# Optimization experiments

Hardware: AMD Instinct MI355X
Metric: run time of the kernel (lower is better)

## Reference

```python
import jax, jax.numpy as jnp
import numpy as np

N, BS, T, D = 512, 64, 200, 32
ALPHA, EPS, TIME_LOG, POWER = 0.1, 1e-6, 5.0, 3


def setup_inputs() -> dict:
    key = jax.random.key(0)
    ks = jax.random.split(key, 16)
    s = 0.1
    skills = jax.random.randint(ks[0], (BS, T), 0, N)
    times = jnp.sort(jax.random.randint(ks[1], (BS, T), 0, 100000), axis=1)
    labels = jax.random.uniform(ks[2], (BS, T), dtype=jnp.float32)
    adj = jax.random.uniform(ks[3], (1, BS, N, N), dtype=jnp.float32)
    node_embeddings = jax.random.normal(ks[4], (1, N, 2 * D), dtype=jnp.float32)
    user_b0 = jax.random.uniform(ks[5], (BS, D), dtype=jnp.float32)
    user_f0 = jax.random.uniform(ks[6], (BS, D), dtype=jnp.float32)
    conv1_w = jax.random.normal(ks[7], (D, D, 5), dtype=jnp.float32) * s
    conv1_b = jax.random.normal(ks[8], (D,), dtype=jnp.float32) * s
    conv2_w = jax.random.normal(ks[9], (D, D, 1), dtype=jnp.float32) * s
    conv2_b = jax.random.normal(ks[10], (D,), dtype=jnp.float32) * s
    lin_f_w = jax.random.normal(ks[11], (D, D), dtype=jnp.float32) * s
    lin_f_b = jax.random.normal(ks[12], (D,), dtype=jnp.float32) * s
    lin_b_w = jax.random.normal(ks[13], (D, D), dtype=jnp.float32) * s
    lin_b_b = jax.random.normal(ks[14], (D,), dtype=jnp.float32) * s
    return dict(skills=skills, times=times, labels=labels, adj=adj,
                node_embeddings=node_embeddings, user_b0=user_b0, user_f0=user_f0,
                conv1_w=conv1_w, conv1_b=conv1_b, conv2_w=conv2_w, conv2_b=conv2_b,
                lin_f_w=lin_f_w, lin_f_b=lin_f_b, lin_b_w=lin_b_w, lin_b_b=lin_b_b)


def _forward(skills, times, labels, adj, node_embeddings, user_b0, user_f0,
             conv1_w, conv1_b, conv2_w, conv2_b, lin_f_w, lin_f_b, lin_b_w, lin_b_b):
    n = jnp.float32(N)
    A1 = adj[0]                      # [BS, N, N]  (leading A=1 dim squeezed)
    A2 = jnp.matmul(A1, A1)
    A3 = jnp.matmul(A2, A1)
    # adj^i / N^i for i=1..3, stacked over power dim -> [BS, 3, N, N]
    adj_list = jnp.stack([A1 / n, A2 / (n * n), A3 / (n * n * n)], axis=1)
    node_emb = node_embeddings[0]    # [N, 2D]
    node_send, node_rec = node_emb[:, :D], node_emb[:, D:]
    # temporal deltas: log(|t_i - t_{i-1}| + EPS) / log(time_log) -> [T-1, BS]
    dt = jnp.abs(times[:, 1:] - times[:, :-1]).astype(jnp.float32)
    delta = (jnp.log(dt + EPS) / jnp.log(jnp.float32(TIME_LOG))).T

    last_perf0 = user_b0 @ node_rec.T           # [BS, N]
    node_last_forget0 = user_f0 @ node_send.T   # [BS, N]

    def step(carry, xs):
        user_b, user_f, last_perf, node_last_forget = carry
        delta_t, label_t, skill_t = xs
        node_cur_base = user_b @ node_rec.T                               # [BS, N]
        temporal = jnp.exp(-delta_t[:, None] * ALPHA * node_last_forget) * last_perf
        # sum over powers folded into the contraction; /(power*N) as in source
        spatial = jnp.einsum('bj,bnjk->bk', last_perf, adj_list) / (POWER * n)
        cur_perf = jax.nn.sigmoid(node_cur_base + temporal + spatial)     # [BS, N]
        nlf = user_f @ node_send.T
        lab = jnp.broadcast_to(label_t[:, None], (BS, D))
        user = jnp.stack([user_b, user_f, lab,
                          node_rec[skill_t], node_send[skill_t]], axis=-1)  # [BS, D, 5]
        h = jax.nn.relu(jnp.einsum('bcl,ocl->bo', user, conv1_w) + conv1_b)
        uu = h @ conv2_w[:, :, 0].T + conv2_b
        new_f = jnp.tanh(uu @ lin_f_w.T + lin_f_b)
        new_b = jnp.tanh(uu @ lin_b_w.T + lin_b_b)
        pred = jnp.take_along_axis(cur_perf, skill_t[:, None], axis=1)    # [BS, 1]
        return (new_b, new_f, cur_perf, nlf), pred

    xs = (delta, labels[:, 1:].T, skills[:, 1:].T)
    _, preds = jax.lax.scan(step, (user_b0, user_f0, last_perf0, node_last_forget0), xs)
    return preds  # [T-1, BS, 1]


def reference(skills, times, labels, adj, node_embeddings, user_b0, user_f0,
              conv1_w, conv1_b, conv2_w, conv2_b, lin_f_w, lin_f_b, lin_b_w, lin_b_b):
    return _forward(skills, times, labels, adj, node_embeddings, user_b0, user_f0,
                    conv1_w, conv1_b, conv2_w, conv2_b, lin_f_w, lin_f_b, lin_b_w, lin_b_b)
```

## Files before the change

### kernel.cpp

```cpp
#include <hip/hip_runtime.h>

#define NN 512
#define BSZ 64
#define TTOT 200
#define NSTEP 199
#define DD 32

typedef __attribute__((ext_vector_type(8))) short bf16x8;
typedef __attribute__((ext_vector_type(8))) int i32x8;
typedef __attribute__((ext_vector_type(4))) float f32x4;
typedef __attribute__((ext_vector_type(4))) unsigned int u32x4;

__device__ __forceinline__ float bf2f(unsigned short u) {
  union { unsigned int i; float f; } v; v.i = ((unsigned int)u) << 16; return v.f;
}
__device__ __forceinline__ unsigned short f2bf(float f) {
  unsigned int b = __float_as_uint(f);
  return (unsigned short)((b + 0x7fffu + ((b >> 16) & 1u)) >> 16);
}
__device__ __forceinline__ unsigned int pk_trunc(float hi, float lo) {
  return __builtin_amdgcn_perm(__float_as_uint(hi), __float_as_uint(lo), 0x07060302u);
}
__device__ __forceinline__ unsigned char e4m3(float x) {
  float a = fabsf(x);
  unsigned int s = (__float_as_uint(x) >> 24) & 0x80u;
  if (a < 0.01171875f) return (unsigned char)s;
  a = fminf(a, 448.0f);
  unsigned int u = __float_as_uint(a);
  unsigned int keep = (u >> 20) & 7u;
  unsigned int rest = u & 0xFFFFFu;
  unsigned int base = (((u >> 23) - 120u) << 3) | keep;
  unsigned int rnd = (rest > 0x80000u) || (rest == 0x80000u && (keep & 1u));
  return (unsigned char)(s | (base + rnd));
}
__device__ __forceinline__ float dec8(unsigned char x) {
  int e = (x >> 3) & 15, m = x & 7;
  float v = e ? ldexpf(8.f + (float)m, e - 10) : ldexpf((float)m, -9);
  return (x & 0x80) ? -v : v;
}
__device__ __forceinline__ float rlane(float v, int l) {
  return __int_as_float(__builtin_amdgcn_readlane(__float_as_int(v), l));
}

__device__ __forceinline__ size_t m8_addr(int k, int col) {
  int nt = col >> 4, cch = k >> 5;
  int l2 = (((k >> 3) & 3) << 4) + (col & 15);
  return (size_t)((nt * 16 + cch) * 512) + (size_t)l2 * 8 + (size_t)(k & 7);
}
__device__ __forceinline__ size_t m8mxa(int k, int col) {
  int f = ((k >> 7) << 5) + (col >> 4);
  int ln2 = (((k >> 5) & 3) << 4) + (col & 15);
  return (((size_t)f * 64 + ln2) << 5) + (size_t)(k & 31);
}

__global__ __launch_bounds__(256) void transpose_kernel(
    const float* __restrict__ A1, unsigned short* __restrict__ A1T) {
  const int b = blockIdx.z, ct = blockIdx.x * 64, rt = blockIdx.y * 64;
  const int t = threadIdx.x;
  __shared__ unsigned int tl[64][33];
  {
    const int rp = t >> 3, cs = (t & 7) * 8;
    const float* p0 = A1 + (size_t)b * NN * NN + (size_t)(rt + 2 * rp) * NN + ct + cs;
    f32x4 a0 = *(const f32x4*)p0, a1 = *(const f32x4*)(p0 + 4);
    f32x4 b0 = *(const f32x4*)(p0 + NN), b1 = *(const f32x4*)(p0 + NN + 4);
#pragma unroll
    for (int j = 0; j < 4; ++j) {
      tl[cs + j][rp] = pk_trunc(b0[j], a0[j]);
      tl[cs + 4 + j][rp] = pk_trunc(b1[j], a1[j]);
    }
  }
  __syncthreads();
  {
    const int c = t >> 2, rps = (t & 3) * 8;
    unsigned int v[8];
#pragma unroll
    for (int j = 0; j < 8; ++j) v[j] = tl[c][rps + j];
    unsigned int* dst = (unsigned int*)(A1T + (size_t)b * NN * NN +
                                        (size_t)(ct + c) * NN + rt) + rps;
    *(u32x4*)dst = u32x4{v[0], v[1], v[2], v[3]};
    *(u32x4*)(dst + 4) = u32x4{v[4], v[5], v[6], v[7]};
  }
}

__global__ __launch_bounds__(256) void gemm_a2_fast(
    const float* __restrict__ A1, const unsigned short* __restrict__ A1T,
    unsigned short* __restrict__ A2) {
  const int tn = blockIdx.x, tm = blockIdx.y, b = blockIdx.z;
  const int tid = threadIdx.x, lane = tid & 63;
  const int w = tid >> 6, wr = w >> 1, wc = w & 1;
  const int q = lane >> 4, ln = lane & 15;
  const size_t Ao = (size_t)b * NN * NN;
  __shared__ __align__(16) unsigned char Asw[128 * 128];
  __shared__ __align__(16) unsigned char Bsw[128 * 128];
  f32x4 acc[4][4];
#pragma unroll
  for (int mi = 0; mi < 4; ++mi)
#pragma unroll
    for (int ni = 0; ni < 4; ++ni) acc[mi][ni] = f32x4{0.f, 0.f, 0.f, 0.f};

  const int arow = tid >> 2, achk = tid & 3;
  const int brow = tid >> 1, bh = tid & 1;
  const float* Ab = A1 + Ao;
  const unsigned short* Bb = A1T + Ao;

  for (int k0 = 0; k0 < NN; k0 += 64) {
#pragma unroll
    for (int p = 0; p < 2; ++p) {
      const int r = arow + p * 64;
      const float* src = Ab + (size_t)(tm * 128 + r) * NN + k0 + achk * 16;
      f32x4 x0 = *(const f32x4*)src, x1 = *(const f32x4*)(src + 4);
      f32x4 x2 = *(const f32x4*)(src + 8), x3 = *(const f32x4*)(src + 12);
      u32x4 y0 = u32x4{pk_trunc(x0[1], x0[0]), pk_trunc(x0[3], x0[2]),
                       pk_trunc(x1[1], x1[0]), pk_trunc(x1[3], x1[2])};
      u32x4 y1 = u32x4{pk_trunc(x2[1], x2[0]), pk_trunc(x2[3], x2[2]),
                       pk_trunc(x3[1], x3[0]), pk_trunc(x3[3], x3[2])};
      const int sw = r & 7;
      *(u32x4*)(Asw + r * 128 + (((achk * 2) ^ sw) << 4)) = y0;
      *(u32x4*)(Asw + r * 128 + (((achk * 2 + 1) ^ sw) << 4)) = y1;
    }
    {
      const unsigned short* src = Bb + (size_t)(tn * 128 + brow) * NN + k0 + bh * 32;
      const int sw = brow & 7;
#pragma unroll
      for (int j = 0; j < 4; ++j) {
        u32x4 v = *(const u32x4*)(src + j * 8);
        *(u32x4*)(Bsw + brow * 128 + (((bh * 4 + j) ^ sw) << 4)) = v;
      }
    }
    __syncthreads();
#pragma unroll
    for (int ks = 0; ks < 2; ++ks) {
      bf16x8 af[4], bv[4];
#pragma unroll
      for (int mi = 0; mi < 4; ++mi) {
        const int r = wr * 64 + mi * 16 + ln;
        af[mi] = *(const bf16x8*)(Asw + r * 128 + (((ks * 4 + q) ^ (r & 7)) << 4));
      }
#pragma unroll
      for (int ni = 0; ni < 4; ++ni) {
        const int r = wc * 64 + ni * 16 + ln;
        bv[ni] = *(const bf16x8*)(Bsw + r * 128 + (((ks * 4 + q) ^ (r & 7)) << 4));
      }
#pragma unroll
      for (int mi = 0; mi < 4; ++mi)
#pragma unroll
        for (int ni = 0; ni < 4; ++ni)
          acc[mi][ni] = __builtin_amdgcn_mfma_f32_16x16x32_bf16(
              af[mi], bv[ni], acc[mi][ni], 0, 0, 0);
    }
    __syncthreads();
  }
  unsigned short* Cb = A2 + Ao;
#pragma unroll
  for (int mi = 0; mi < 4; ++mi)
#pragma unroll
    for (int ni = 0; ni < 4; ++ni) {
      const int col = tn * 128 + wc * 64 + ni * 16 + ln;
#pragma unroll
      for (int r = 0; r < 4; ++r) {
        const int row = tm * 128 + wr * 64 + mi * 16 + q * 4 + r;
        Cb[(size_t)row * NN + col] = f2bf(acc[mi][ni][r]);
      }
    }
}

__global__ __launch_bounds__(256) void gemm_m_fast(
    const float* __restrict__ A1, const unsigned short* __restrict__ A1T,
    const unsigned short* __restrict__ A2, unsigned char* __restrict__ M8k,
    unsigned char* __restrict__ M8x, int has_mx) {
  const int tn = blockIdx.x, tm = blockIdx.y, b = blockIdx.z;
  const int tid = threadIdx.x, lane = tid & 63;
  const int w = tid >> 6, wr = w >> 1, wc = w & 1;
  const int q = lane >> 4, ln = lane & 15;
  const size_t Ao = (size_t)b * NN * NN;
  __shared__ __align__(16) unsigned char Asw[128 * 128];
  __shared__ __align__(16) unsigned char Bsw[128 * 128];
  f32x4 acc[4][4];
#pragma unroll
  for (int mi = 0; mi < 4; ++mi)
#pragma unroll
    for (int ni = 0; ni < 4; ++ni) acc[mi][ni] = f32x4{0.f, 0.f, 0.f, 0.f};

  const int srow = tid >> 1, sh = tid & 1;
  const unsigned short* A2b = A2 + Ao;
  const unsigned short* Bb = A1T + Ao;

  for (int k0 = 0; k0 < NN; k0 += 64) {
    {
      const unsigned short* asrc = A2b + (size_t)(tm * 128 + srow) * NN + k0 + sh * 32;
      const unsigned short* bsrc = Bb + (size_t)(tn * 128 + srow) * NN + k0 + sh * 32;
      const int sw = srow & 7;
#pragma unroll
      for (int j = 0; j < 4; ++j) {
        u32x4 va = *(const u32x4*)(asrc + j * 8);
        u32x4 vb = *(const u32x4*)(bsrc + j * 8);
        *(u32x4*)(Asw + srow * 128 + (((sh * 4 + j) ^ sw) << 4)) = va;
        *(u32x4*)(Bsw + srow * 128 + (((sh * 4 + j) ^ sw) << 4)) = vb;
      }
    }
    __syncthreads();
#pragma unroll
    for (int ks = 0; ks < 2; ++ks) {
      bf16x8 af[4], bv[4];
#pragma unroll
      for (int mi = 0; mi < 4; ++mi) {
        const int r = wr * 64 + mi * 16 + ln;
        af[mi] = *(const bf16x8*)(Asw + r * 128 + (((ks * 4 + q) ^ (r & 7)) << 4));
      }
#pragma unroll
      for (int ni = 0; ni < 4; ++ni) {
        const int r = wc * 64 + ni * 16 + ln;
        bv[ni] = *(const bf16x8*)(Bsw + r * 128 + (((ks * 4 + q) ^ (r & 7)) << 4));
      }
#pragma unroll
      for (int mi = 0; mi < 4; ++mi)
#pragma unroll
        for (int ni = 0; ni < 4; ++ni)
          acc[mi][ni] = __builtin_amdgcn_mfma_f32_16x16x32_bf16(
              af[mi], bv[ni], acc[mi][ni], 0, 0, 0);
    }
    __syncthreads();
  }
  const float c1 = 1048576.f / (3.f * 512.f * 512.f);
  const float c2 = c1 / 512.f;
  const float c3 = c2 / 512.f;
  unsigned char* Mk = M8k + Ao;
  unsigned char* Mx = M8x + Ao;
#pragma unroll
  for (int mi = 0; mi < 4; ++mi) {
    const int row0 = tm * 128 + wr * 64 + mi * 16 + q * 4;
#pragma unroll
    for (int ni = 0; ni < 4; ++ni) {
      const int col = tn * 128 + wc * 64 + ni * 16 + ln;
      unsigned int wv = 0;
#pragma unroll
      for (int r = 0; r < 4; ++r) {
        const int row = row0 + r;
        float mval = c1 * A1[Ao + (size_t)row * NN + col] +
                     c2 * bf2f(A2b[(size_t)row * NN + col]) + c3 * acc[mi][ni][r];
        wv |= ((unsigned int)e4m3(mval)) << (8 * r);
      }
      *(unsigned int*)(Mk + m8_addr(row0, col)) = wv;
      if (has_mx) *(unsigned int*)(Mx + m8mxa(row0, col)) = wv;
    }
  }
}

__global__ __launch_bounds__(256) void gemm_a2_slow(
    const float* __restrict__ A1, unsigned short* __restrict__ A2) {
  const int b = blockIdx.x, tn = blockIdx.y, tm = blockIdx.z;
  const int tid = threadIdx.x, lane = tid & 63, w = tid >> 6;
  const int q = lane >> 4, ln = lane & 15;
  const size_t Ao = (size_t)b * NN * NN;
  f32x4 zero = {0.f, 0.f, 0.f, 0.f};
  f32x4 acc[4] = {zero, zero, zero, zero};
  const float* ap = A1 + Ao + (size_t)(tm * 64 + w * 16 + ln) * NN + q * 8;
  for (int k0 = 0; k0 < NN; k0 += 32) {
    f32x4 x0 = *(const f32x4*)(ap + k0);
    f32x4 x1 = *(const f32x4*)(ap + k0 + 4);
    union { bf16x8 v; unsigned int u[4]; } af;
    af.u[0] = pk_trunc(x0[1], x0[0]);
    af.u[1] = pk_trunc(x0[3], x0[2]);
    af.u[2] = pk_trunc(x1[1], x1[0]);
    af.u[3] = pk_trunc(x1[3], x1[2]);
#pragma unroll
    for (int i = 0; i < 4; ++i) {
      bf16x8 bv;
#pragma unroll
      for (int j = 0; j < 8; ++j)
        bv[j] = (short)f2bf(A1[Ao + (size_t)(k0 + q * 8 + j) * NN + tn * 64 + i * 16 + ln]);
      acc[i] = __builtin_amdgcn_mfma_f32_16x16x32_bf16(af.v, bv, acc[i], 0, 0, 0);
    }
  }
  unsigned short* Cb = A2 + Ao;
#pragma unroll
  for (int i = 0; i < 4; ++i) {
    int col = tn * 64 + i * 16 + ln;
#pragma unroll
    for (int r = 0; r < 4; ++r) {
      int row = tm * 64 + w * 16 + q * 4 + r;
      Cb[(size_t)row * NN + col] = f2bf(acc[i][r]);
    }
  }
}

__global__ __launch_bounds__(256) void gemm_m_slow(
    const float* __restrict__ A1, const unsigned short* __restrict__ A2,
    unsigned char* __restrict__ M8k, unsigned char* __restrict__ M8x,
    int has_mx) {
  const int b = blockIdx.x, tn = blockIdx.y, tm = blockIdx.z;
  const int tid = threadIdx.x, lane = tid & 63, w = tid >> 6;
  const int q = lane >> 4, ln = lane & 15;
  const size_t Ao = (size_t)b * NN * NN;
  const unsigned short* A2b = A2 + Ao;
  f32x4 zero = {0.f, 0.f, 0.f, 0.f};
  f32x4 acc[4] = {zero, zero, zero, zero};
  const unsigned short* ap = A2b + (size_t)(tm * 64 + w * 16 + ln) * NN + q * 8;
  for (int k0 = 0; k0 < NN; k0 += 32) {
    bf16x8 af = *(const bf16x8*)(ap + k0);
#pragma unroll
    for (int i = 0; i < 4; ++i) {
      bf16x8 bv;
#pragma unroll
      for (int j = 0; j < 8; ++j)
        bv[j] = (short)f2bf(A1[Ao + (size_t)(k0 + q * 8 + j) * NN + tn * 64 + i * 16 + ln]);
      acc[i] = __builtin_amdgcn_mfma_f32_16x16x32_bf16(af, bv, acc[i], 0, 0, 0);
    }
  }
  const float c1 = 1048576.f / (3.f * 512.f * 512.f);
  const float c2 = c1 / 512.f;
  const float c3 = c2 / 512.f;
  unsigned char* Mk = M8k + Ao;
  unsigned char* Mx = M8x + Ao;
  const int row0 = tm * 64 + w * 16 + q * 4;
#pragma unroll
  for (int i = 0; i < 4; ++i) {
    int col = tn * 64 + i * 16 + ln;
    unsigned int wv = 0;
#pragma unroll
    for (int r = 0; r < 4; ++r) {
      int row = row0 + r;
      float mval = c1 * A1[Ao + (size_t)row * NN + col] +
                   c2 * bf2f(A2b[(size_t)row * NN + col]) + c3 * acc[i][r];
      wv |= ((unsigned int)e4m3(mval)) << (8 * r);
    }
    *(unsigned int*)(Mk + m8_addr(row0, col)) = wv;
    if (has_mx) *(unsigned int*)(Mx + m8mxa(row0, col)) = wv;
  }
}

__global__ __launch_bounds__(64) void probe_kernel(int* __restrict__ flag) {
  const int lane = threadIdx.x, q = lane >> 4, n = lane & 15;
  __shared__ unsigned char A8[128];
  __shared__ unsigned char B8[128 * 16];
  for (int k = lane; k < 128; k += 64) A8[k] = (unsigned char)(8 + ((k * 37 + 11) % 56));
  for (int i = lane; i < 2048; i += 64)
    B8[i] = (unsigned char)(((i & 1) ? 0x80 : 0) | (8 + ((i * 23 + 5) % 56)));
  __syncthreads();
  union { i32x8 v; unsigned char b[32]; } af, bf;
#pragma unroll
  for (int j = 0; j < 32; ++j) {
    af.b[j] = A8[q * 32 + j];
    bf.b[j] = B8[(q * 32 + j) * 16 + n];
  }
  f32x4 acc = {0.f, 0.f, 0.f, 0.f};
  acc = __builtin_amdgcn_mfma_scale_f32_16x16x128_f8f6f4(af.v, bf.v, acc, 0, 0,
                                                         0, 127, 0, 127);
  float ref = 0.f;
  for (int k = 0; k < 128; ++k) ref += dec8(A8[k]) * dec8(B8[k * 16 + n]);
  int ok = 1;
#pragma unroll
  for (int r = 0; r < 4; ++r)
    ok &= (fabsf(acc[r] - ref) <= 1e-3f * fmaxf(fabsf(ref), 1.f)) ? 1 : 0;
  unsigned long long bal = __ballot(ok);
  if (lane == 0) *flag = (bal == ~0ull) ? 1 : 0;
}

__global__ __launch_bounds__(64, 1) void traj3_kernel(
    const int* __restrict__ skills, const float* __restrict__ labels,
    const float* __restrict__ emb, const float* __restrict__ ub0g,
    const float* __restrict__ uf0g, const float* __restrict__ w1g,
    const float* __restrict__ b1g, const float* __restrict__ w2g,
    const float* __restrict__ b2g, const float* __restrict__ wfg,
    const float* __restrict__ bfg, const float* __restrict__ wbg,
    const float* __restrict__ bbg, float* __restrict__ UBg,
    float* __restrict__ UFg) {
  const int b = blockIdx.x;
  const int lane = threadIdx.x;
  const int o = lane & 31, half = lane >> 5;

  __shared__ float label_s[NSTEP];
  __shared__ int skill_s[NSTEP];
  for (int i = lane; i < NSTEP; i += 64) {
    label_s[i] = labels[b * TTOT + i + 1];
    skill_s[i] = skills[b * TTOT + i + 1];
  }

  float w1r[160];
#pragma unroll
  for (int i = 0; i < 40; ++i) {
    f32x4 v = *(const f32x4*)(w1g + o * 160 + i * 4);
    w1r[i * 4 + 0] = v[0]; w1r[i * 4 + 1] = v[1];
    w1r[i * 4 + 2] = v[2]; w1r[i * 4 + 3] = v[3];
  }
  float w2r[32];
#pragma unroll
  for (int i = 0; i < 8; ++i) {
    f32x4 v = *(const f32x4*)(w2g + o * 32 + i * 4);
    w2r[i * 4 + 0] = v[0]; w2r[i * 4 + 1] = v[1];
    w2r[i * 4 + 2] = v[2]; w2r[i * 4 + 3] = v[3];
  }
  const float* wsg = half ? wbg : wfg;
  float wsr[32];
#pragma unroll
  for (int i = 0; i < 8; ++i) {
    f32x4 v = *(const f32x4*)(wsg + o * 32 + i * 4);
    wsr[i * 4 + 0] = v[0]; wsr[i * 4 + 1] = v[1];
    wsr[i * 4 + 2] = v[2]; wsr[i * 4 + 3] = v[3];
  }
  const float b1r = b1g[o], b2r = b2g[o];
  const float bselr = half ? bbg[o] : bfg[o];

  float val = half ? ub0g[b * DD + o] : uf0g[b * DD + o];

  __syncthreads();

  float* UBp = UBg + (size_t)b * NSTEP * DD;
  float* UFp = UFg + (size_t)b * NSTEP * DD;

  float evc = emb[(size_t)skill_s[0] * (2 * DD) + lane];
  float labc = label_s[0];
  float pgA[8], pgB[8];

  for (int step = 0; step < NSTEP; ++step) {
    float evn = 0.f, labn = 0.f;
    if (step + 1 < NSTEP) {
      evn = emb[(size_t)skill_s[step + 1] * (2 * DD) + lane];
      labn = label_s[step + 1];
    }
    if (step) {
      float partA = pgA[0];
#pragma unroll
      for (int k = 1; k < 8; ++k) partA += pgA[k];
      float partB = pgB[0];
#pragma unroll
      for (int k = 1; k < 8; ++k) partB += pgB[k];
      float h = b1r + partA + partB;
      h = fmaxf(h, 0.f);
      float up_a = 0.f, up_b = 0.f;
#pragma unroll
      for (int cc = 0; cc < 16; ++cc) {
        up_a += rlane(h, cc) * w2r[cc];
        up_b += rlane(h, 16 + cc) * w2r[16 + cc];
      }
      float uu = b2r + up_a + up_b;
      float aac = bselr;
#pragma unroll
      for (int c = 0; c < DD; ++c) aac += rlane(uu, c) * wsr[c];
      val = 1.f - 2.f / (1.f + __expf(2.f * aac));
    }
    (half ? UBp : UFp)[step * DD + o] = val;
#pragma unroll
    for (int k = 0; k < 8; ++k) {
      {
        const int c0 = 2 * k;
        float ubc0 = rlane(val, 32 + c0), ubc1 = rlane(val, 33 + c0);
        float ufc0 = rlane(val, c0), ufc1 = rlane(val, c0 + 1);
        float rs0 = rlane(evc, c0), rs1 = rlane(evc, c0 + 1);
        float rr0 = rlane(evc, 32 + c0), rr1 = rlane(evc, 33 + c0);
        float hpart = ubc0 * w1r[c0 * 5 + 0] + ufc0 * w1r[c0 * 5 + 1] +
                      labc * w1r[c0 * 5 + 2] + rr0 * w1r[c0 * 5 + 3] +
                      rs0 * w1r[c0 * 5 + 4];
        hpart += ubc1 * w1r[(c0 + 1) * 5 + 0] + ufc1 * w1r[(c0 + 1) * 5 + 1] +
                 labc * w1r[(c0 + 1) * 5 + 2] + rr1 * w1r[(c0 + 1) * 5 + 3] +
                 rs1 * w1r[(c0 + 1) * 5 + 4];
        pgA[k] = hpart;
      }
      {
        const int c0 = 16 + 2 * k;
        float ubc0 = rlane(val, 32 + c0), ubc1 = rlane(val, 33 + c0);
        float ufc0 = rlane(val, c0), ufc1 = rlane(val, c0 + 1);
        float rs0 = rlane(evc, c0), rs1 = rlane(evc, c0 + 1);
        float rr0 = rlane(evc, 32 + c0), rr1 = rlane(evc, 33 + c0);
        float hpart = ubc0 * w1r[c0 * 5 + 0] + ufc0 * w1r[c0 * 5 + 1] +
                      labc * w1r[c0 * 5 + 2] + rr0 * w1r[c0 * 5 + 3] +
                      rs0 * w1r[c0 * 5 + 4];
        hpart += ubc1 * w1r[(c0 + 1) * 5 + 0] + ufc1 * w1r[(c0 + 1) * 5 + 1] +
                 labc * w1r[(c0 + 1) * 5 + 2] + rr1 * w1r[(c0 + 1) * 5 + 3] +
                 rs1 * w1r[(c0 + 1) * 5 + 4];
        pgB[k] = hpart;
      }
    }
    evc = evn;
    labc = labn;
  }
}

__global__ __launch_bounds__(512) void precomp_kernel(
    const int* __restrict__ times, const float* __restrict__ emb,
    const float* __restrict__ UBg, const float* __restrict__ UFg,
    float* __restrict__ NCBg, float* __restrict__ TCg) {
  const int b = blockIdx.x;
  const int s0 = blockIdx.y * 8;
  const int n = threadIdx.x;
  float nr[DD], ns[DD];
#pragma unroll
  for (int c = 0; c < DD; ++c) {
    ns[c] = emb[(size_t)n * (2 * DD) + c];
    nr[c] = emb[(size_t)n * (2 * DD) + DD + c];
  }
  for (int s = s0; s < s0 + 8 && s < NSTEP; ++s) {
    const float* ubp = UBg + ((size_t)b * NSTEP + s) * DD;
    const float* ufp = UFg + ((size_t)b * NSTEP + (s ? s - 1 : 0)) * DD;
    float n0 = 0.f, n1 = 0.f, n2 = 0.f, n3 = 0.f;
    float l0 = 0.f, l1 = 0.f, l2 = 0.f, l3 = 0.f;
#pragma unroll
    for (int c = 0; c < 8; ++c) {
      n0 += ubp[c] * nr[c];
      n1 += ubp[8 + c] * nr[8 + c];
      n2 += ubp[16 + c] * nr[16 + c];
      n3 += ubp[24 + c] * nr[24 + c];
      l0 += ufp[c] * ns[c];
      l1 += ufp[8 + c] * ns[8 + c];
      l2 += ufp[16 + c] * ns[16 + c];
      l3 += ufp[24 + c] * ns[24 + c];
    }
    float ncb = (n0 + n1) + (n2 + n3);
    float nlf = (l0 + l1) + (l2 + l3);
    int dt_ = times[b * TTOT + s + 1] - times[b * TTOT + s];
    if (dt_ < 0) dt_ = -dt_;
    float delta = __logf((float)dt_ + 1e-6f) * 0.6213349345596119f;
    float tc = __expf(-delta * 0.1f * nlf);
    NCBg[((size_t)b * NSTEP + s) * NN + n] = ncb;
    TCg[((size_t)b * NSTEP + s) * NN + n] = tc;
  }
}

__global__ __launch_bounds__(512, 2) void scan_fast(
    const int* __restrict__ skills, const float* __restrict__ NCBg,
    const float* __restrict__ TCg, const unsigned char* __restrict__ M8k,
    const unsigned char* __restrict__ M8x, int allow_mx,
    const int* __restrict__ flag, float* __restrict__ out) {
  const int b = blockIdx.x;
  const int t = threadIdx.x;
  const int lane = t & 63, w = t >> 6, q = lane >> 4;
  __shared__ __align__(32) unsigned char lp8[2][NN];
  __shared__ int skill_s[NSTEP];
  const int use_mx = allow_mx && (*flag);
  for (int i = t; i < NSTEP; i += 512) skill_s[i] = skills[b * TTOT + i + 1];

  union MU { i32x8 v; long l[4]; };
  MU mreg[16];
  if (use_mx) {
    const unsigned char* Mb = M8x + (size_t)b * NN * NN;
#pragma unroll
    for (int c = 0; c < 4; ++c)
#pragma unroll
      for (int i = 0; i < 4; ++i)
        mreg[c * 4 + i].v = *(const i32x8*)(
            Mb + (((size_t)(c * 32 + w * 4 + i) * 64 + lane) << 5));
  } else {
    const unsigned char* Mb = M8k + (size_t)b * NN * NN;
#pragma unroll
    for (int c = 0; c < 16; ++c)
#pragma unroll
      for (int i = 0; i < 4; ++i)
        mreg[c].l[i] = *(const long*)(
            Mb + (((size_t)(w * 64 + i * 16 + c)) << 9) + (size_t)lane * 8);
  }
  const float* ncbp = NCBg + (size_t)b * NSTEP * NN + t;
  const float* tcp = TCg + (size_t)b * NSTEP * NN + t;
  float ncb_c = ncbp[0];
  float tc_c = tcp[0];
  float rlp = ncb_c;
  lp8[0][t] = e4m3(rlp);
  __syncthreads();

  int pidx = -1;
// ... 148 lines not shown
      for (int c = 0; c < DD; ++c) aac += rlane(uu, c) * wsel[c * 32 + o];
      float val = 1.f - 2.f / (1.f + __expf(2.f * aac));
      if (half) ub[o] = val;
      else uf[o] = val;
    }
    f32x4 zero = {0.f, 0.f, 0.f, 0.f};
    f32x4 acc[4] = {zero, zero, zero, zero};
    if (use_mx) {
#pragma unroll
      for (int c = 0; c < 4; ++c) {
        i32x8 af = *(const i32x8*)(&lp8[c * 128 + q * 32]);
#pragma unroll
        for (int i = 0; i < 4; ++i)
          acc[i] = __builtin_amdgcn_mfma_scale_f32_16x16x128_f8f6f4(
              af, mreg[c * 4 + i].v, acc[i], 0, 0, 0, 127, 0, 127);
      }
    } else {
#pragma unroll
      for (int c = 0; c < 16; ++c) {
        long af = *(const long*)(&lp8[c * 32 + q * 8]);
#pragma unroll
        for (int i = 0; i < 4; ++i)
          acc[i] = __builtin_amdgcn_mfma_f32_16x16x32_fp8_fp8(af, mreg[c].l[i],
                                                              acc[i], 0, 0, 0);
      }
    }
    float spatial = ((q & 2) ? ((q & 1) ? acc[3][0] : acc[2][0])
                             : ((q & 1) ? acc[1][0] : acc[0][0])) * 0x1p-20f;
    __syncthreads();

    float rub = ub[lane & 31], ruf = uf[lane & 31];
    float n0 = 0.f, n1 = 0.f, n2 = 0.f, n3 = 0.f;
    float l0 = 0.f, l1 = 0.f, l2 = 0.f, l3 = 0.f;
#pragma unroll
    for (int c = 0; c < 8; ++c) {
      n0 += rlane(rub, c) * nrec[c];
      n1 += rlane(rub, 8 + c) * nrec[8 + c];
      n2 += rlane(rub, 16 + c) * nrec[16 + c];
      n3 += rlane(rub, 24 + c) * nrec[24 + c];
      l0 += rlane(ruf, c) * nsend[c];
      l1 += rlane(ruf, 8 + c) * nsend[8 + c];
      l2 += rlane(ruf, 16 + c) * nsend[16 + c];
      l3 += rlane(ruf, 24 + c) * nsend[24 + c];
    }
    float ncb = (n0 + n1) + (n2 + n3);
    float nlfn = (l0 + l1) + (l2 + l3);
    float e = __expf(-delta_s[step] * 0.1f * rnlf) * rlp;
    float cur = 1.f / (1.f + __expf(-(ncb + e + spatial)));

    {
      int o = t & 31, s = t >> 5;
      float lab = label_s[step];
      int sk = skill_s[step];
      float hpart = 0.f;
#pragma unroll
      for (int cc = 0; cc < 2; ++cc) {
        int c = (s << 1) + cc;
        const float* wrow = &w1t[(c * 5) * 32 + o];
        float rs = emb[(size_t)sk * (2 * DD) + c];
        float rr = emb[(size_t)sk * (2 * DD) + DD + c];
        hpart += ub[c] * wrow[0] + uf[c] * wrow[32] + lab * wrow[64] +
                 rr * wrow[96] + rs * wrow[128];
      }
      hp[s][o] = hpart;
    }

    rlp = cur;
    rnlf = nlfn;
    lp8[t] = e4m3(cur);
    if (t == skill_s[step]) out[step * BSZ + b] = cur;
    __syncthreads();
  }
}

extern "C" void kernel_launch(void* const* d_in, const int* in_sizes, int n_in,
                              void* d_out, int out_size, void* d_ws, size_t ws_size,
                              hipStream_t stream) {
  (void)in_sizes; (void)n_in; (void)out_size;
  const int* skills = (const int*)d_in[0];
  const int* times = (const int*)d_in[1];
  const float* labels = (const float*)d_in[2];
  const float* adj = (const float*)d_in[3];
  const float* emb = (const float*)d_in[4];

  const size_t mat = (size_t)BSZ * NN * NN;
  const size_t ncb_sz = (size_t)BSZ * NSTEP * NN * sizeof(float);
  const size_t ub_sz = (size_t)BSZ * NSTEP * DD * sizeof(float);
  char* base = (char*)d_ws;
  unsigned char *M8k, *M8x;
  unsigned short *A2, *A1T = nullptr;
  char* ovl = nullptr;
  int* flag;
  int use_fast, allow_mx;
  if (ws_size >= 6 * mat + 4) {
    use_fast = 1; allow_mx = 1;
    M8k = (unsigned char*)base; M8x = M8k + mat;
    A2 = (unsigned short*)(base + 2 * mat);
    A1T = (unsigned short*)(base + 4 * mat);
    flag = (int*)(base + 6 * mat);
    ovl = base + 2 * mat;
  } else if (ws_size >= 5 * mat + 4) {
    use_fast = 1; allow_mx = 0;
    M8k = (unsigned char*)base; M8x = M8k;
    A2 = (unsigned short*)(base + mat);
    A1T = (unsigned short*)(base + 3 * mat);
    flag = (int*)(base + 5 * mat);
    ovl = base + mat;
  } else if (ws_size >= 4 * mat + 4) {
    use_fast = 0; allow_mx = 1;
    M8k = (unsigned char*)base; M8x = M8k + mat;
    A2 = (unsigned short*)(base + 2 * mat);
    flag = (int*)(base + 4 * mat);
  } else {
    use_fast = 0; allow_mx = 0;
    M8k = (unsigned char*)base; M8x = M8k;
    A2 = (unsigned short*)(base + mat);
    flag = (int*)(base + 3 * mat);
  }

  dim3 gb(256);
  if (use_fast) {
    dim3 gt(8, 8, BSZ);
    dim3 gf(4, 4, BSZ);
    transpose_kernel<<<gt, gb, 0, stream>>>(adj, A1T);
    gemm_a2_fast<<<gf, gb, 0, stream>>>(adj, A1T, A2);
    gemm_m_fast<<<gf, gb, 0, stream>>>(adj, A1T, A2, M8k, M8x, allow_mx);
    float* NCB = (float*)ovl;
    float* TC = (float*)(ovl + ncb_sz);
    float* UB = (float*)(ovl + 2 * ncb_sz);
    float* UF = (float*)(ovl + 2 * ncb_sz + ub_sz);
    traj3_kernel<<<dim3(BSZ), dim3(64), 0, stream>>>(
        skills, labels, emb, (const float*)d_in[5], (const float*)d_in[6],
        (const float*)d_in[7], (const float*)d_in[8], (const float*)d_in[9],
        (const float*)d_in[10], (const float*)d_in[11], (const float*)d_in[12],
        (const float*)d_in[13], (const float*)d_in[14], UB, UF);
    precomp_kernel<<<dim3(BSZ, 25), dim3(512), 0, stream>>>(times, emb, UB, UF,
                                                            NCB, TC);
    probe_kernel<<<dim3(1), dim3(64), 0, stream>>>(flag);
    scan_fast<<<dim3(BSZ), dim3(512), 0, stream>>>(skills, NCB, TC, M8k, M8x,
                                                   allow_mx, flag, (float*)d_out);
  } else {
    dim3 gg(BSZ, 8, 8);
    gemm_a2_slow<<<gg, gb, 0, stream>>>(adj, A2);
    gemm_m_slow<<<gg, gb, 0, stream>>>(adj, A2, M8k, M8x, allow_mx);
    probe_kernel<<<dim3(1), dim3(64), 0, stream>>>(flag);
    scan_kernel<<<dim3(BSZ), dim3(512), 0, stream>>>(
        skills, times, labels, emb, (const float*)d_in[5], (const float*)d_in[6],
        (const float*)d_in[7], (const float*)d_in[8], (const float*)d_in[9],
        (const float*)d_in[10], (const float*)d_in[11], (const float*)d_in[12],
        (const float*)d_in[13], (const float*)d_in[14], M8k, M8x, allow_mx, flag,
        (float*)d_out);
  }
}
```

Baseline: 651.5 us.

## Overlap serial trajectory recurrence with GEMM kernels via extra side blocks

The serial per-batch user-state recurrence (traj3) is split into three chunks, and each chunk runs in extra blocks attached to the transpose, A2 GEMM and M GEMM launches. State is checkpointed to workspace between chunks, so the latency-bound recurrence hides behind the bandwidth- and compute-bound matrix work instead of running as its own serial launch. The MX-layout copy of M8 is moved out of the GEMM epilogue into a separate relayout kernel. The W1 weights move from registers to transposed shared memory. The workspace is reshuffled so these buffers fit. Each chunk still runs serially on one wave, so the extra blocks may lengthen the tail of the GEMM launches.

```diff
diff --git a/kernel.cpp b/kernel.cpp
--- a/kernel.cpp
+++ b/kernel.cpp
@@ -5,6 +5,8 @@
 #define TTOT 200
 #define NSTEP 199
 #define DD 32
+#define CHK1 66
+#define CHK2 132
 
 typedef __attribute__((ext_vector_type(8))) short bf16x8;
 typedef __attribute__((ext_vector_type(8))) int i32x8;
@@ -53,11 +55,160 @@
   return (((size_t)f * 64 + ln2) << 5) + (size_t)(k & 31);
 }
 
-__global__ __launch_bounds__(256) void transpose_kernel(
-    const float* __restrict__ A1, unsigned short* __restrict__ A1T) {
+__device__ __forceinline__ void traj_steps(
+    int b, int s_begin, int s_end, int lane, float* w1t, float* label_s,
+    int* skill_s, const int* __restrict__ skills,
+    const float* __restrict__ labels, const float* __restrict__ emb,
+    const float* __restrict__ ub0g, const float* __restrict__ uf0g,
+    const float* __restrict__ w1g, const float* __restrict__ b1g,
+    const float* __restrict__ w2g, const float* __restrict__ b2g,
+    const float* __restrict__ wfg, const float* __restrict__ bfg,
+    const float* __restrict__ wbg, const float* __restrict__ bbg,
+    float* __restrict__ UBg, float* __restrict__ UFg, float* __restrict__ CKg) {
+  const int o = lane & 31, half = lane >> 5;
+  for (int idx = lane; idx < DD * 5 * DD; idx += 64) {
+    int oo = idx / 160, rem = idx % 160;
+    w1t[rem * 32 + oo] = w1g[idx];
+  }
+  for (int i = lane; i < NSTEP; i += 64) {
+    label_s[i] = labels[b * TTOT + i + 1];
+    skill_s[i] = skills[b * TTOT + i + 1];
+  }
+  float w2r[32];
+#pragma unroll
+  for (int i = 0; i < 8; ++i) {
+    f32x4 v = *(const f32x4*)(w2g + o * 32 + i * 4);
+    w2r[i * 4 + 0] = v[0]; w2r[i * 4 + 1] = v[1];
+    w2r[i * 4 + 2] = v[2]; w2r[i * 4 + 3] = v[3];
+  }
+  const float* wsg = half ? wbg : wfg;
+  float wsr[32];
+#pragma unroll
+  for (int i = 0; i < 8; ++i) {
+    f32x4 v = *(const f32x4*)(wsg + o * 32 + i * 4);
+    wsr[i * 4 + 0] = v[0]; wsr[i * 4 + 1] = v[1];
+    wsr[i * 4 + 2] = v[2]; wsr[i * 4 + 3] = v[3];
+  }
+  const float b1r = b1g[o], b2r = b2g[o];
+  const float bselr = half ? bbg[o] : bfg[o];
+
+  float val, pgA[8], pgB[8];
+  float* ck = CKg + ((size_t)b * 64 + lane) * 17;
+  if (s_begin == 0) {
+    val = half ? ub0g[b * DD + o] : uf0g[b * DD + o];
+  } else {
+    val = ck[0];
+#pragma unroll
+    for (int k = 0; k < 8; ++k) { pgA[k] = ck[1 + k]; pgB[k] = ck[9 + k]; }
+  }
+  float* UBp = UBg + (size_t)b * NSTEP * DD;
+  float* UFp = UFg + (size_t)b * NSTEP * DD;
+
+  float evc = emb[(size_t)skill_s[s_begin] * (2 * DD) + lane];
+  float labc = label_s[s_begin];
+
+  for (int step = s_begin; step < s_end; ++step) {
+    float evn = 0.f, labn = 0.f;
+    if (step + 1 < NSTEP) {
+      evn = emb[(size_t)skill_s[step + 1] * (2 * DD) + lane];
+      labn = label_s[step + 1];
+    }
+    if (step) {
+      float partA = pgA[0];
+#pragma unroll
+      for (int k = 1; k < 8; ++k) partA += pgA[k];
+      float partB = pgB[0];
+#pragma unroll
+      for (int k = 1; k < 8; ++k) partB += pgB[k];
+      float h = b1r + partA + partB;
+      h = fmaxf(h, 0.f);
+      float up_a = 0.f, up_b = 0.f;
+#pragma unroll
+      for (int cc = 0; cc < 16; ++cc) {
+        up_a += rlane(h, cc) * w2r[cc];
+        up_b += rlane(h, 16 + cc) * w2r[16 + cc];
+      }
+      float uu = b2r + up_a + up_b;
+      float aac = bselr;
+#pragma unroll
+      for (int c = 0; c < DD; ++c) aac += rlane(uu, c) * wsr[c];
+      val = 1.f - 2.f / (1.f + __expf(2.f * aac));
+    }
+    (half ? UBp : UFp)[step * DD + o] = val;
+#pragma unroll
+    for (int k = 0; k < 8; ++k) {
+      {
+        const int c0 = 2 * k;
+        float ubc0 = rlane(val, 32 + c0), ubc1 = rlane(val, 33 + c0);
+        float ufc0 = rlane(val, c0), ufc1 = rlane(val, c0 + 1);
+        float rs0 = rlane(evc, c0), rs1 = rlane(evc, c0 + 1);
+        float rr0 = rlane(evc, 32 + c0), rr1 = rlane(evc, 33 + c0);
+        float hpart = ubc0 * w1t[(c0 * 5 + 0) * 32 + o] +
+                      ufc0 * w1t[(c0 * 5 + 1) * 32 + o] +
+                      labc * w1t[(c0 * 5 + 2) * 32 + o] +
+                      rr0 * w1t[(c0 * 5 + 3) * 32 + o] +
+                      rs0 * w1t[(c0 * 5 + 4) * 32 + o];
+        hpart += ubc1 * w1t[((c0 + 1) * 5 + 0) * 32 + o] +
+                 ufc1 * w1t[((c0 + 1) * 5 + 1) * 32 + o] +
+                 labc * w1t[((c0 + 1) * 5 + 2) * 32 + o] +
+                 rr1 * w1t[((c0 + 1) * 5 + 3) * 32 + o] +
+                 rs1 * w1t[((c0 + 1) * 5 + 4) * 32 + o];
+        pgA[k] = hpart;
+      }
+      {
+        const int c0 = 16 + 2 * k;
+        float ubc0 = rlane(val, 32 + c0), ubc1 = rlane(val, 33 + c0);
+        float ufc0 = rlane(val, c0), ufc1 = rlane(val, c0 + 1);
+        float rs0 = rlane(evc, c0), rs1 = rlane(evc, c0 + 1);
+        float rr0 = rlane(evc, 32 + c0), rr1 = rlane(evc, 33 + c0);
+        float hpart = ubc0 * w1t[(c0 * 5 + 0) * 32 + o] +
+                      ufc0 * w1t[(c0 * 5 + 1) * 32 + o] +
+                      labc * w1t[(c0 * 5 + 2) * 32 + o] +
+                      rr0 * w1t[(c0 * 5 + 3) * 32 + o] +
+                      rs0 * w1t[(c0 * 5 + 4) * 32 + o];
+        hpart += ubc1 * w1t[((c0 + 1) * 5 + 0) * 32 + o] +
+                 ufc1 * w1t[((c0 + 1) * 5 + 1) * 32 + o] +
+                 labc * w1t[((c0 + 1) * 5 + 2) * 32 + o] +
+                 rr1 * w1t[((c0 + 1) * 5 + 3) * 32 + o] +
+                 rs1 * w1t[((c0 + 1) * 5 + 4) * 32 + o];
+        pgB[k] = hpart;
+      }
+    }
+    evc = evn;
+    labc = labn;
+  }
+  if (s_end < NSTEP) {
+    ck[0] = val;
+#pragma unroll
+    for (int k = 0; k < 8; ++k) { ck[1 + k] = pgA[k]; ck[9 + k] = pgB[k]; }
+  }
+}
+
+#define TRAJ_ARGS                                                              \
+  const int *skills, const float *labels_t, const float *emb_t,                \
+      const float *ub0g, const float *uf0g, const float *w1g,                  \
+      const float *b1g, const float *w2g, const float *b2g, const float *wfg,  \
+      const float *bfg, const float *wbg, const float *bbg, float *UBg,        \
+      float *UFg, float *CKg
+#define TRAJ_PASS                                                              \
+  skills, labels_t, emb_t, ub0g, uf0g, w1g, b1g, w2g, b2g, wfg, bfg, wbg,      \
+      bbg, UBg, UFg, CKg
+
+__global__ __launch_bounds__(256) void transpose_traj(
+    const float* __restrict__ A1, unsigned short* __restrict__ A1T,
+    TRAJ_ARGS) {
+  __shared__ __align__(16) unsigned char smem[22080];
+  const int t = threadIdx.x;
+  if (blockIdx.x == 8) {
+    if (blockIdx.y != 0 || t >= 64) return;
+    float* w1t = (float*)smem;
+    float* label_s = (float*)(smem + 20480);
+    int* skill_s = (int*)(smem + 20480 + 800);
+    traj_steps(blockIdx.z, 0, CHK1, t, w1t, label_s, skill_s, TRAJ_PASS);
+    return;
+  }
   const int b = blockIdx.z, ct = blockIdx.x * 64, rt = blockIdx.y * 64;
-  const int t = threadIdx.x;
-  __shared__ unsigned int tl[64][33];
+  unsigned int(*tl)[33] = (unsigned int(*)[33])smem;
   {
     const int rp = t >> 3, cs = (t & 7) * 8;
     const float* p0 = A1 + (size_t)b * NN * NN + (size_t)(rt + 2 * rp) * NN + ct + cs;
@@ -84,14 +235,24 @@
 
 __global__ __launch_bounds__(256) void gemm_a2_fast(
     const float* __restrict__ A1, const unsigned short* __restrict__ A1T,
-    unsigned short* __restrict__ A2) {
+    unsigned short* __restrict__ A2, TRAJ_ARGS) {
+  __shared__ __align__(16) unsigned char smem[32768];
+  const int tid = threadIdx.x;
+  if (blockIdx.x == 4) {
+    if (blockIdx.y != 0 || tid >= 64) return;
+    float* w1t = (float*)smem;
+    float* label_s = (float*)(smem + 20480);
+    int* skill_s = (int*)(smem + 20480 + 800);
+    traj_steps(blockIdx.z, CHK1, CHK2, tid, w1t, label_s, skill_s, TRAJ_PASS);
+    return;
+  }
   const int tn = blockIdx.x, tm = blockIdx.y, b = blockIdx.z;
-  const int tid = threadIdx.x, lane = tid & 63;
+  const int lane = tid & 63;
   const int w = tid >> 6, wr = w >> 1, wc = w & 1;
   const int q = lane >> 4, ln = lane & 15;
   const size_t Ao = (size_t)b * NN * NN;
-  __shared__ __align__(16) unsigned char Asw[128 * 128];
-  __shared__ __align__(16) unsigned char Bsw[128 * 128];
+  unsigned char* Asw = smem;
+  unsigned char* Bsw = smem + 128 * 128;
   f32x4 acc[4][4];
 #pragma unroll
   for (int mi = 0; mi < 4; ++mi)
@@ -167,14 +328,24 @@
 __global__ __launch_bounds__(256) void gemm_m_fast(
     const float* __restrict__ A1, const unsigned short* __restrict__ A1T,
     const unsigned short* __restrict__ A2, unsigned char* __restrict__ M8k,
-    unsigned char* __restrict__ M8x, int has_mx) {
+    TRAJ_ARGS) {
+  __shared__ __align__(16) unsigned char smem[32768];
+  const int tid = threadIdx.x;
+  if (blockIdx.x == 4) {
+    if (blockIdx.y != 0 || tid >= 64) return;
+    float* w1t = (float*)smem;
+    float* label_s = (float*)(smem + 20480);
+    int* skill_s = (int*)(smem + 20480 + 800);
+    traj_steps(blockIdx.z, CHK2, NSTEP, tid, w1t, label_s, skill_s, TRAJ_PASS);
+    return;
+  }
   const int tn = blockIdx.x, tm = blockIdx.y, b = blockIdx.z;
-  const int tid = threadIdx.x, lane = tid & 63;
+  const int lane = tid & 63;
   const int w = tid >> 6, wr = w >> 1, wc = w & 1;
   const int q = lane >> 4, ln = lane & 15;
   const size_t Ao = (size_t)b * NN * NN;
-  __shared__ __align__(16) unsigned char Asw[128 * 128];
-  __shared__ __align__(16) unsigned char Bsw[128 * 128];
+  unsigned char* Asw = smem;
+  unsigned char* Bsw = smem + 128 * 128;
   f32x4 acc[4][4];
 #pragma unroll
   for (int mi = 0; mi < 4; ++mi)
@@ -225,7 +396,6 @@
   const float c2 = c1 / 512.f;
   const float c3 = c2 / 512.f;
   unsigned char* Mk = M8k + Ao;
-  unsigned char* Mx = M8x + Ao;
 #pragma unroll
   for (int mi = 0; mi < 4; ++mi) {
     const int row0 = tm * 128 + wr * 64 + mi * 16 + q * 4;
@@ -241,8 +411,23 @@
         wv |= ((unsigned int)e4m3(mval)) << (8 * r);
       }
       *(unsigned int*)(Mk + m8_addr(row0, col)) = wv;
-      if (has_mx) *(unsigned int*)(Mx + m8mxa(row0, col)) = wv;
-    }
+    }
+  }
+}
+
+__global__ __launch_bounds__(256) void mx_relayout(
+    const unsigned char* __restrict__ M8k, unsigned char* __restrict__ M8x) {
+  const int b = blockIdx.x;
+  const int t0 = blockIdx.y * 256 + threadIdx.x;
+  const unsigned char* src = M8k + (size_t)b * NN * NN;
+  unsigned char* dst = M8x + (size_t)b * NN * NN;
+#pragma unroll
+  for (int j = 0; j < 8; ++j) {
+    int idx = t0 + j * 8192;
+    int r4 = idx & 127, col = idx >> 7;
+    int row0 = r4 * 4;
+    *(unsigned int*)(dst + m8mxa(row0, col)) =
+        *(const unsigned int*)(src + m8_addr(row0, col));
   }
 }
 
@@ -356,124 +541,13 @@
   if (lane == 0) *flag = (bal == ~0ull) ? 1 : 0;
 }
 
-__global__ __launch_bounds__(64, 1) void traj3_kernel(
-    const int* __restrict__ skills, const float* __restrict__ labels,
-    const float* __restrict__ emb, const float* __restrict__ ub0g,
-    const float* __restrict__ uf0g, const float* __restrict__ w1g,
-    const float* __restrict__ b1g, const float* __restrict__ w2g,
-    const float* __restrict__ b2g, const float* __restrict__ wfg,
-    const float* __restrict__ bfg, const float* __restrict__ wbg,
-    const float* __restrict__ bbg, float* __restrict__ UBg,
-    float* __restrict__ UFg) {
-  const int b = blockIdx.x;
+__global__ __launch_bounds__(64, 1) void traj3_kernel(TRAJ_ARGS) {
+  __shared__ __align__(16) unsigned char smem[22080];
   const int lane = threadIdx.x;
-  const int o = lane & 31, half = lane >> 5;
-
-  __shared__ float label_s[NSTEP];
-  __shared__ int skill_s[NSTEP];
-  for (int i = lane; i < NSTEP; i += 64) {
-    label_s[i] = labels[b * TTOT + i + 1];
-    skill_s[i] = skills[b * TTOT + i + 1];
-  }
-
-  float w1r[160];
-#pragma unroll
-  for (int i = 0; i < 40; ++i) {
-    f32x4 v = *(const f32x4*)(w1g + o * 160 + i * 4);
-    w1r[i * 4 + 0] = v[0]; w1r[i * 4 + 1] = v[1];
-    w1r[i * 4 + 2] = v[2]; w1r[i * 4 + 3] = v[3];
-  }
-  float w2r[32];
-#pragma unroll
-  for (int i = 0; i < 8; ++i) {
-    f32x4 v = *(const f32x4*)(w2g + o * 32 + i * 4);
-    w2r[i * 4 + 0] = v[0]; w2r[i * 4 + 1] = v[1];
-    w2r[i * 4 + 2] = v[2]; w2r[i * 4 + 3] = v[3];
-  }
-  const float* wsg = half ? wbg : wfg;
-  float wsr[32];
-#pragma unroll
-  for (int i = 0; i < 8; ++i) {
-    f32x4 v = *(const f32x4*)(wsg + o * 32 + i * 4);
-    wsr[i * 4 + 0] = v[0]; wsr[i * 4 + 1] = v[1];
-    wsr[i * 4 + 2] = v[2]; wsr[i * 4 + 3] = v[3];
-  }
-  const float b1r = b1g[o], b2r = b2g[o];
-  const float bselr = half ? bbg[o] : bfg[o];
-
-  float val = half ? ub0g[b * DD + o] : uf0g[b * DD + o];
-
-  __syncthreads();
-
-  float* UBp = UBg + (size_t)b * NSTEP * DD;
-  float* UFp = UFg + (size_t)b * NSTEP * DD;
-
-  float evc = emb[(size_t)skill_s[0] * (2 * DD) + lane];
-  float labc = label_s[0];
-  float pgA[8], pgB[8];
-
-  for (int step = 0; step < NSTEP; ++step) {
-    float evn = 0.f, labn = 0.f;
-    if (step + 1 < NSTEP) {
-      evn = emb[(size_t)skill_s[step + 1] * (2 * DD) + lane];
-      labn = label_s[step + 1];
-    }
-    if (step) {
-      float partA = pgA[0];
-#pragma unroll
-      for (int k = 1; k < 8; ++k) partA += pgA[k];
-      float partB = pgB[0];
-#pragma unroll
-      for (int k = 1; k < 8; ++k) partB += pgB[k];
-      float h = b1r + partA + partB;
-      h = fmaxf(h, 0.f);
-      float up_a = 0.f, up_b = 0.f;
-#pragma unroll
-      for (int cc = 0; cc < 16; ++cc) {
-        up_a += rlane(h, cc) * w2r[cc];
-        up_b += rlane(h, 16 + cc) * w2r[16 + cc];
-      }
-      float uu = b2r + up_a + up_b;
-      float aac = bselr;
-#pragma unroll
-      for (int c = 0; c < DD; ++c) aac += rlane(uu, c) * wsr[c];
-      val = 1.f - 2.f / (1.f + __expf(2.f * aac));
-    }
-    (half ? UBp : UFp)[step * DD + o] = val;
-#pragma unroll
-    for (int k = 0; k < 8; ++k) {
-      {
-        const int c0 = 2 * k;
-        float ubc0 = rlane(val, 32 + c0), ubc1 = rlane(val, 33 + c0);
-        float ufc0 = rlane(val, c0), ufc1 = rlane(val, c0 + 1);
-        float rs0 = rlane(evc, c0), rs1 = rlane(evc, c0 + 1);
-        float rr0 = rlane(evc, 32 + c0), rr1 = rlane(evc, 33 + c0);
-        float hpart = ubc0 * w1r[c0 * 5 + 0] + ufc0 * w1r[c0 * 5 + 1] +
-                      labc * w1r[c0 * 5 + 2] + rr0 * w1r[c0 * 5 + 3] +
-                      rs0 * w1r[c0 * 5 + 4];
-        hpart += ubc1 * w1r[(c0 + 1) * 5 + 0] + ufc1 * w1r[(c0 + 1) * 5 + 1] +
-                 labc * w1r[(c0 + 1) * 5 + 2] + rr1 * w1r[(c0 + 1) * 5 + 3] +
-                 rs1 * w1r[(c0 + 1) * 5 + 4];
-        pgA[k] = hpart;
-      }
-      {
-        const int c0 = 16 + 2 * k;
-        float ubc0 = rlane(val, 32 + c0), ubc1 = rlane(val, 33 + c0);
-        float ufc0 = rlane(val, c0), ufc1 = rlane(val, c0 + 1);
-        float rs0 = rlane(evc, c0), rs1 = rlane(evc, c0 + 1);
-        float rr0 = rlane(evc, 32 + c0), rr1 = rlane(evc, 33 + c0);
-        float hpart = ubc0 * w1r[c0 * 5 + 0] + ufc0 * w1r[c0 * 5 + 1] +
-                      labc * w1r[c0 * 5 + 2] + rr0 * w1r[c0 * 5 + 3] +
-                      rs0 * w1r[c0 * 5 + 4];
-        hpart += ubc1 * w1r[(c0 + 1) * 5 + 0] + ufc1 * w1r[(c0 + 1) * 5 + 1] +
-                 labc * w1r[(c0 + 1) * 5 + 2] + rr1 * w1r[(c0 + 1) * 5 + 3] +
-                 rs1 * w1r[(c0 + 1) * 5 + 4];
-        pgB[k] = hpart;
-      }
-    }
-    evc = evn;
-    labc = labn;
-  }
+  float* w1t = (float*)smem;
+  float* label_s = (float*)(smem + 20480);
+  int* skill_s = (int*)(smem + 20480 + 800);
+  traj_steps(blockIdx.x, 0, NSTEP, lane, w1t, label_s, skill_s, TRAJ_PASS);
 }
 
 __global__ __launch_bounds__(512) void precomp_kernel(
@@ -788,73 +862,100 @@
   const float* labels = (const float*)d_in[2];
   const float* adj = (const float*)d_in[3];
   const float* emb = (const float*)d_in[4];
+  const float* ub0 = (const float*)d_in[5];
+  const float* uf0 = (const float*)d_in[6];
+  const float* w1 = (const float*)d_in[7];
+  const float* b1 = (const float*)d_in[8];
+  const float* w2 = (const float*)d_in[9];
+  const float* b2 = (const float*)d_in[10];
+  const float* wf = (const float*)d_in[11];
+  const float* bf = (const float*)d_in[12];
+  const float* wb = (const float*)d_in[13];
+  const float* bb = (const float*)d_in[14];
 
   const size_t mat = (size_t)BSZ * NN * NN;
   const size_t ncb_sz = (size_t)BSZ * NSTEP * NN * sizeof(float);
   const size_t ub_sz = (size_t)BSZ * NSTEP * DD * sizeof(float);
   char* base = (char*)d_ws;
-  unsigned char *M8k, *M8x;
-  unsigned short *A2, *A1T = nullptr;
-  char* ovl = nullptr;
-  int* flag;
-  int use_fast, allow_mx;
+  dim3 gb(256);
+
   if (ws_size >= 6 * mat + 4) {
-    use_fast = 1; allow_mx = 1;
-    M8k = (unsigned char*)base; M8x = M8k + mat;
-    A2 = (unsigned short*)(base + 2 * mat);
-    A1T = (unsigned short*)(base + 4 * mat);
-    flag = (int*)(base + 6 * mat);
-    ovl = base + 2 * mat;
+    unsigned char* M8k = (unsigned char*)base;
+    unsigned short* A1T = (unsigned short*)(base + 1 * mat);
+    unsigned short* A2 = (unsigned short*)(base + 3 * mat);
+    unsigned char* M8x = (unsigned char*)(base + 5 * mat);
+    int* flag = (int*)(base + 6 * mat);
+    float* UB = (float*)(base + 5 * mat);
+    float* UF = (float*)(base + 5 * mat + ub_sz);
+    float* CK = (float*)(base + 5 * mat + 2 * ub_sz);
+    float* NCB = (float*)(base + 1 * mat);
+    float* TC = (float*)(base + 1 * mat + ncb_sz);
+
+    transpose_traj<<<dim3(9, 8, BSZ), gb, 0, stream>>>(
+        adj, A1T, skills, labels, emb, ub0, uf0, w1, b1, w2, b2, wf, bf, wb,
+        bb, UB, UF, CK);
+    gemm_a2_fast<<<dim3(5, 4, BSZ), gb, 0, stream>>>(
+        adj, A1T, A2, skills, labels, emb, ub0, uf0, w1, b1, w2, b2, wf, bf,
+        wb, bb, UB, UF, CK);
+    gemm_m_fast<<<dim3(5, 4, BSZ), gb, 0, stream>>>(
+        adj, A1T, A2, M8k, skills, labels, emb, ub0, uf0, w1, b1, w2, b2, wf,
+        bf, wb, bb, UB, UF, CK);
+    precomp_kernel<<<dim3(BSZ, 25), dim3(512), 0, stream>>>(times, emb, UB, UF,
+                                                            NCB, TC);
+    mx_relayout<<<dim3(BSZ, 32), gb, 0, stream>>>(M8k, M8x);
+    probe_kernel<<<dim3(1), dim3(64), 0, stream>>>(flag);
+    scan_fast<<<dim3(BSZ), dim3(512), 0, stream>>>(skills, NCB, TC, M8k, M8x,
+                                                   1, flag, (float*)d_out);
   } else if (ws_size >= 5 * mat + 4) {
-    use_fast = 1; allow_mx = 0;
-    M8k = (unsigned char*)base; M8x = M8k;
-    A2 = (unsigned short*)(base + mat);
-    A1T = (unsigned short*)(base + 3 * mat);
-    flag = (int*)(base + 5 * mat);
-    ovl = base + mat;
-  } else if (ws_size >= 4 * mat + 4) {
-    use_fast = 0; allow_mx = 1;
-    M8k = (unsigned char*)base; M8x = M8k + mat;
-    A2 = (unsigned short*)(base + 2 * mat);
-    flag = (int*)(base + 4 * mat);
-  } else {
-    use_fast = 0; allow_mx = 0;
-    M8k = (unsigned char*)base; M8x = M8k;
-    A2 = (unsigned short*)(base + mat);
-    flag = (int*)(base + 3 * mat);
-  }
-
-  dim3 gb(256);
-  if (use_fast) {
-    dim3 gt(8, 8, BSZ);
-    dim3 gf(4, 4, BSZ);
-    transpose_kernel<<<gt, gb, 0, stream>>>(adj, A1T);
-    gemm_a2_fast<<<gf, gb, 0, stream>>>(adj, A1T, A2);
-    gemm_m_fast<<<gf, gb, 0, stream>>>(adj, A1T, A2, M8k, M8x, allow_mx);
-    float* NCB = (float*)ovl;
-    float* TC = (float*)(ovl + ncb_sz);
-    float* UB = (float*)(ovl + 2 * ncb_sz);
-    float* UF = (float*)(ovl + 2 * ncb_sz + ub_sz);
+    unsigned char* M8k = (unsigned char*)base;
+    unsigned short* A1T = (unsigned short*)(base + 1 * mat);
+    unsigned short* A2 = (unsigned short*)(base + 3 * mat);
+    int* flag = (int*)(base + 5 * mat);
+    float* NCB = (float*)(base + 1 * mat);
+    float* TC = (float*)(base + 1 * mat + ncb_sz);
+    float* UB = (float*)(base + 1 * mat + 2 * ncb_sz);
+    float* UF = (float*)(base + 1 * mat + 2 * ncb_sz + ub_sz);
+    float* CK = (float*)(base + 1 * mat + 2 * ncb_sz + 2 * ub_sz);
+
+    transpose_traj<<<dim3(8, 8, BSZ), gb, 0, stream>>>(
+        adj, A1T, skills, labels, emb, ub0, uf0, w1, b1, w2, b2, wf, bf, wb,
+        bb, UB, UF, CK);
+    gemm_a2_fast<<<dim3(4, 4, BSZ), gb, 0, stream>>>(
+        adj, A1T, A2, skills, labels, emb, ub0, uf0, w1, b1, w2, b2, wf, bf,
+        wb, bb, UB, UF, CK);
+    gemm_m_fast<<<dim3(4, 4, BSZ), gb, 0, stream>>>(
+        adj, A1T, A2, M8k, skills, labels, emb, ub0, uf0, w1, b1, w2, b2, wf,
+        bf, wb, bb, UB, UF, CK);
     traj3_kernel<<<dim3(BSZ), dim3(64), 0, stream>>>(
-        skills, labels, emb, (const float*)d_in[5], (const float*)d_in[6],
-        (const float*)d_in[7], (const float*)d_in[8], (const float*)d_in[9],
-        (const float*)d_in[10], (const float*)d_in[11], (const float*)d_in[12],
-        (const float*)d_in[13], (const float*)d_in[14], UB, UF);
+        skills, labels, emb, ub0, uf0, w1, b1, w2, b2, wf, bf, wb, bb, UB, UF,
+        CK);
     precomp_kernel<<<dim3(BSZ, 25), dim3(512), 0, stream>>>(times, emb, UB, UF,
                                                             NCB, TC);
     probe_kernel<<<dim3(1), dim3(64), 0, stream>>>(flag);
-    scan_fast<<<dim3(BSZ), dim3(512), 0, stream>>>(skills, NCB, TC, M8k, M8x,
-                                                   allow_mx, flag, (float*)d_out);
-  } else {
+    scan_fast<<<dim3(BSZ), dim3(512), 0, stream>>>(skills, NCB, TC, M8k, M8k,
+                                                   0, flag, (float*)d_out);
+  } else if (ws_size >= 4 * mat + 4) {
+    unsigned char* M8k = (unsigned char*)base;
+    unsigned char* M8x = M8k + mat;
+    unsigned short* A2 = (unsigned short*)(base + 2 * mat);
+    int* flag = (int*)(base + 4 * mat);
     dim3 gg(BSZ, 8, 8);
     gemm_a2_slow<<<gg, gb, 0, stream>>>(adj, A2);
-    gemm_m_slow<<<gg, gb, 0, stream>>>(adj, A2, M8k, M8x, allow_mx);
+    gemm_m_slow<<<gg, gb, 0, stream>>>(adj, A2, M8k, M8x, 1);
     probe_kernel<<<dim3(1), dim3(64), 0, stream>>>(flag);
     scan_kernel<<<dim3(BSZ), dim3(512), 0, stream>>>(
-        skills, times, labels, emb, (const float*)d_in[5], (const float*)d_in[6],
-        (const float*)d_in[7], (const float*)d_in[8], (const float*)d_in[9],
-        (const float*)d_in[10], (const float*)d_in[11], (const float*)d_in[12],
-        (const float*)d_in[13], (const float*)d_in[14], M8k, M8x, allow_mx, flag,
-        (float*)d_out);
-  }
-}
+        skills, times, labels, emb, ub0, uf0, w1, b1, w2, b2, wf, bf, wb, bb,
+        M8k, M8x, 1, flag, (float*)d_out);
+  } else {
+    unsigned char* M8k = (unsigned char*)base;
+    unsigned short* A2 = (unsigned short*)(base + mat);
+    int* flag = (int*)(base + 3 * mat);
+    dim3 gg(BSZ, 8, 8);
+    gemm_a2_slow<<<gg, gb, 0, stream>>>(adj, A2);
+    gemm_m_slow<<<gg, gb, 0, stream>>>(adj, A2, M8k, M8k, 0);
+    probe_kernel<<<dim3(1), dim3(64), 0, stream>>>(flag);
+    scan_kernel<<<dim3(BSZ), dim3(512), 0, stream>>>(
+        skills, times, labels, emb, ub0, uf0, w1, b1, w2, b2, wf, bf, wb, bb,
+        M8k, M8k, 0, flag, (float*)d_out);
+  }
+}
```

Result: slower. 937.9 us (+44.0%).
